# Kernel optimization log

Measured on AMD Instinct MI355X. Metric: run time of the kernel, lower is better.

The kernel has to match this reference:

```python
import jax, jax.numpy as jnp
import numpy as np

N = 2048        # rows of input (nodes / samples)
D_IN = 1024     # input_dim
D_OUT = 8192    # output_dim == number of rows/cols of sparse adj
E = 131072      # nnz of adj (avg degree 16 over D_OUT)


def setup_inputs() -> dict:
    key = jax.random.key(0)
    k0, k1, k2, k3, k4 = jax.random.split(key, 5)
    inp = jax.random.normal(k0, (N, D_IN), dtype=jnp.float32)
    # kaiming_uniform_ on [D_IN, D_OUT]: bound = sqrt(6 / fan_in)
    bound = float(np.sqrt(6.0 / D_IN))
    weight = jax.random.uniform(k1, (D_IN, D_OUT), dtype=jnp.float32,
                                minval=-bound, maxval=bound)
    bias = jnp.zeros((D_OUT,), dtype=jnp.float32)
    adj_rows = jax.random.randint(k2, (E,), 0, D_OUT, dtype=jnp.int64)
    adj_cols = jax.random.randint(k3, (E,), 0, D_OUT, dtype=jnp.int64)
    adj_vals = jax.random.uniform(k4, (E,), dtype=jnp.float32)
    return {"input": inp, "weight": weight, "bias": bias,
            "adj_rows": adj_rows, "adj_cols": adj_cols, "adj_vals": adj_vals}


def reference(input, weight, bias, adj_rows, adj_cols, adj_vals):
    # support = input @ W                      -> [N, D_OUT]
    support = jnp.matmul(input, weight)
    # torch.sparse.mm(adj, support.T).T == (adj @ support^T)^T,
    # with adj sparse COO [D_OUT, D_OUT]: result[r, :] += val_e * support[:, col_e]
    support_t = support.T                      # [D_OUT, N]
    msgs = adj_vals[:, None] * support_t[adj_cols]          # [E, N]
    agg = jax.ops.segment_sum(msgs, adj_rows, num_segments=D_OUT)  # [D_OUT, N]
    return agg.T + bias                        # [N, D_OUT]
```

## Files before the change

### kernel.cpp

```cpp
#include <hip/hip_runtime.h>
#include <hip/hip_bf16.h>


#define N_ROWS 2048
#define D_IN   1024
#define D_OUT  8192
#define SLOT_SHIFT 6
#define SLOTS (1 << SLOT_SHIFT)

typedef __attribute__((ext_vector_type(8))) short bf16x8;
typedef __attribute__((ext_vector_type(4))) float f32x4;
typedef __attribute__((ext_vector_type(2))) float f32x2;

__device__ __forceinline__ float bf2f(unsigned short u) {
    union { unsigned int i; float f; } x; x.i = ((unsigned int)u) << 16; return x.f;
}
__device__ __forceinline__ unsigned short f2bf(float f) {
    union { unsigned int i; float f; } x; x.f = f;
    unsigned int r = x.i + 0x7FFFu + ((x.i >> 16) & 1u);
    return (unsigned short)(r >> 16);
}

__device__ __forceinline__ void async_load16(const void* g, void* l) {
    __builtin_amdgcn_global_load_lds(
        (const __attribute__((address_space(1))) void*)g,
        (__attribute__((address_space(3))) void*)l,
        16, 0, 0);
}

__global__ __launch_bounds__(256) void fused_pre(
    const float* __restrict__ w, unsigned short* __restrict__ wt,
    const float* __restrict__ in, unsigned short* __restrict__ xout,
    const int* __restrict__ rows, const int* __restrict__ cols,
    const float* __restrict__ vals,
    int* __restrict__ cursors, int2* __restrict__ csr_cv, int E)
{
    __shared__ float tile[64][65];
    const int b = blockIdx.x;
    const int t = threadIdx.x;

    if (b < 2048) {
        const int bx = b & 127;
        const int by = b >> 7;
        #pragma unroll
        for (int pass = 0; pass < 4; ++pass) {
            const int item = pass * 256 + t;
            const int r  = item >> 4;
            const int c4 = item & 15;
            const float4 v = *(const float4*)&w[(size_t)(by * 64 + r) * D_OUT + bx * 64 + c4 * 4];
            tile[r][c4 * 4 + 0] = v.x; tile[r][c4 * 4 + 1] = v.y;
            tile[r][c4 * 4 + 2] = v.z; tile[r][c4 * 4 + 3] = v.w;
        }
        __syncthreads();
        #pragma unroll
        for (int pass = 0; pass < 4; ++pass) {
            const int item = pass * 256 + t;
            const int rr  = item >> 4;
            const int cc4 = item & 15;
            ushort4 o;
            o.x = f2bf(tile[cc4 * 4 + 0][rr]);
            o.y = f2bf(tile[cc4 * 4 + 1][rr]);
            o.z = f2bf(tile[cc4 * 4 + 2][rr]);
            o.w = f2bf(tile[cc4 * 4 + 3][rr]);
            *(ushort4*)&wt[(size_t)(bx * 64 + rr) * D_IN + by * 64 + cc4 * 4] = o;
        }
    } else if (b < 4096) {
        const int i = ((b - 2048) * 256 + t) * 4;
        const float4 v = *(const float4*)(in + i);
        ushort4 o; o.x = f2bf(v.x); o.y = f2bf(v.y); o.z = f2bf(v.z); o.w = f2bf(v.w);
        *(ushort4*)(xout + i) = o;
    } else {
        const int e = (b - 4096) * 256 + t;
        if (e < E) {
            const int r = rows[e];
            const int pos = atomicAdd(&cursors[r], 1);
            if (pos < SLOTS) {
                int2 cv; cv.x = cols[e]; cv.y = __float_as_int(vals[e]);
                csr_cv[(r << SLOT_SHIFT) + pos] = cv;
            }
        }
    }
}

__global__ __launch_bounds__(256, 8) void aggregate_slices(
    const unsigned short* __restrict__ wtb,
    const int* __restrict__ cnts,
    const int2* __restrict__ csr_cv,
    unsigned short* __restrict__ wpt)
{
    const int wave  = threadIdx.x >> 6;
    const int lane  = threadIdx.x & 63;
    const int slice = blockIdx.x & 7;
    const int r     = (blockIdx.x >> 3) * 4 + wave;
    const int k0    = slice * 128 + lane * 2;

    const int beg = r << SLOT_SHIFT;
    int cnt = cnts[r]; if (cnt > SLOTS) cnt = SLOTS;
    const int end = beg + cnt;

    const unsigned short* wb = wtb + k0;
    f32x2 acc = (f32x2){0.f, 0.f};

    int i = beg;
    for (; i + 4 <= end; i += 4) {
        int2 cv[4]; unsigned int g[4];
        #pragma unroll
        for (int j = 0; j < 4; ++j) cv[j] = csr_cv[i + j];
        #pragma unroll
        for (int j = 0; j < 4; ++j)
            g[j] = *(const unsigned int*)(wb + (size_t)cv[j].x * D_IN);
        #pragma unroll
        for (int j = 0; j < 4; ++j) {
            const float v = __int_as_float(cv[j].y);
            union { unsigned int i; float f; } lo, hi;
            lo.i = g[j] << 16; hi.i = g[j] & 0xffff0000u;
            acc += (f32x2){v, v} * (f32x2){lo.f, hi.f};
        }
    }
    for (; i < end; ++i) {
        const int2 cv = csr_cv[i];
        const float v = __int_as_float(cv.y);
        const unsigned int g = *(const unsigned int*)(wb + (size_t)cv.x * D_IN);
        union { unsigned int i; float f; } lo, hi;
        lo.i = g << 16; hi.i = g & 0xffff0000u;
        acc += (f32x2){v, v} * (f32x2){lo.f, hi.f};
    }

    const unsigned int o = (unsigned int)f2bf(acc[0]) | ((unsigned int)f2bf(acc[1]) << 16);
    *(unsigned int*)(wpt + (size_t)r * D_IN + k0) = o;
}

struct QuadFrags { bf16x8 a00, a01, a10, a11; };

#define READQ_G(Q, AK, MI0)                                                     \
    (Q).a00 = *(const bf16x8*)((AK) + (MI0)     * 16384);                       \
    (Q).a01 = *(const bf16x8*)((AK) + (MI0)     * 16384 + 32);                  \
    (Q).a10 = *(const bf16x8*)((AK) + (MI0 + 1) * 16384);                       \
    (Q).a11 = *(const bf16x8*)((AK) + (MI0 + 1) * 16384 + 32);

#define READ_BFR(BASE)                                                          \
    _Pragma("unroll")                                                           \
    for (int ni = 0; ni < 4; ++ni) {                                            \
        bfr[0][ni] = *(const bf16x8*)((BASE) + rowB + ni * 1024 + x0 * 8);      \
        bfr[1][ni] = *(const bf16x8*)((BASE) + rowB + ni * 1024 + x1 * 8);      \
    }

#define MFMA_Q(Q, MI0)                                                          \
    __builtin_amdgcn_s_setprio(1);                                              \
    _Pragma("unroll")                                                           \
    for (int ni = 0; ni < 4; ++ni)                                              \
        acc[MI0][ni]     = __builtin_amdgcn_mfma_f32_16x16x32_bf16(             \
            (Q).a00, bfr[0][ni], acc[MI0][ni], 0, 0, 0);                        \
    _Pragma("unroll")                                                           \
    for (int ni = 0; ni < 4; ++ni)                                              \
        acc[MI0 + 1][ni] = __builtin_amdgcn_mfma_f32_16x16x32_bf16(             \
            (Q).a10, bfr[0][ni], acc[MI0 + 1][ni], 0, 0, 0);                    \
    _Pragma("unroll")                                                           \
    for (int ni = 0; ni < 4; ++ni)                                              \
        acc[MI0][ni]     = __builtin_amdgcn_mfma_f32_16x16x32_bf16(             \
            (Q).a01, bfr[1][ni], acc[MI0][ni], 0, 0, 0);                        \
    _Pragma("unroll")                                                           \
    for (int ni = 0; ni < 4; ++ni)                                              \
        acc[MI0 + 1][ni] = __builtin_amdgcn_mfma_f32_16x16x32_bf16(             \
            (Q).a11, bfr[1][ni], acc[MI0 + 1][ni], 0, 0, 0);                    \
    __builtin_amdgcn_s_setprio(0);

__global__ __launch_bounds__(512, 2) void gemm_bt_bias(
    const unsigned short* __restrict__ A,
    const unsigned short* __restrict__ B,
    const float*  __restrict__ bias,
    float* __restrict__ C)
{
    __shared__ unsigned short lds[32768];

    const int tid  = threadIdx.x;
    const int wave = tid >> 6;
    const int lane = tid & 63;
    const int q    = lane >> 4;
    const int l16  = lane & 15;
    const int wr   = wave >> 2;
    const int wc   = wave & 3;

    const int bc = blockIdx.x;
    const int br = blockIdx.y;

    const int srow = tid >> 3;
    const int lc   = (tid & 7) ^ (srow & 7);
    const char* Bsrc = (const char*)B + ((size_t)(bc * 256) + srow) * (D_IN * 2) + lc * 16;
    char* ldsc = (char*)lds;

    const int x0   = q ^ (l16 & 7);
    const int x1   = x0 ^ 4;
    const int rowB = (wc * 64 + l16) * 64;

    const unsigned short* aA =
        A + (size_t)(br * 256 + wr * 128 + l16) * D_IN + q * 8;

    f32x4 acc[8][4];
    #pragma unroll
    for (int i = 0; i < 8; ++i)
        #pragma unroll
        for (int j = 0; j < 4; ++j)
            acc[i][j] = (f32x4){0.f, 0.f, 0.f, 0.f};

    #pragma unroll
    for (int j = 0; j < 4; ++j)
        async_load16(Bsrc + (size_t)j * 64 * (D_IN * 2), ldsc + j * 8192 + tid * 16);

    asm volatile("s_waitcnt vmcnt(0)" ::: "memory");
    __builtin_amdgcn_s_barrier();

    QuadFrags RA, RB;
    bf16x8 bfr[2][4];
    {
        READ_BFR(lds)
        READQ_G(RA, aA, 0)
    }

    for (int kt = 0; kt < D_IN / 64; ++kt) {
        const int cur = kt & 1;
        const unsigned short* Bb = lds + cur * 16384;
        char* dstB = ldsc + (cur ^ 1) * 32768 + tid * 16;
        const char* srcB = Bsrc + (size_t)(kt + 1) * 128;
        const unsigned short* aK = aA + kt * 64;
        const bool pf = (kt + 1 < D_IN / 64);

        if (pf) {
            async_load16(srcB,                            dstB);
            async_load16(srcB + (size_t)64  * (D_IN * 2), dstB + 8192);
            async_load16(srcB + (size_t)128 * (D_IN * 2), dstB + 16384);
            async_load16(srcB + (size_t)192 * (D_IN * 2), dstB + 24576);
        }
        READQ_G(RB, aK, 2)
        MFMA_Q(RA, 0)

        READQ_G(RA, aK, 4)
        MFMA_Q(RB, 2)

        READQ_G(RB, aK, 6)
        MFMA_Q(RA, 4)

        if (pf) {
            asm volatile("s_waitcnt vmcnt(0) lgkmcnt(0)" ::: "memory");
            __builtin_amdgcn_s_barrier();
            READQ_G(RA, aK + 64, 0)
            MFMA_Q(RB, 6)
            READ_BFR(lds + (cur ^ 1) * 16384)
        } else {
            MFMA_Q(RB, 6)
        }
    }

    #pragma unroll
    for (int ni = 0; ni < 4; ++ni) {
        const int col = bc * 256 + wc * 64 + ni * 16 + l16;
        const float bv = bias[col];
        #pragma unroll
        for (int mi = 0; mi < 8; ++mi) {
            const int row0 = br * 256 + wr * 128 + mi * 16 + q * 4;
            #pragma unroll
            for (int r = 0; r < 4; ++r)
                C[(size_t)(row0 + r) * D_OUT + col] = acc[mi][ni][r] + bv;
        }
    }
}

extern "C" void kernel_launch(void* const* d_in, const int* in_sizes, int n_in,
                              void* d_out, int out_size, void* d_ws, size_t ws_size,
                              hipStream_t stream) {
    (void)n_in; (void)out_size; (void)ws_size;
    const float* input    = (const float*)d_in[0];
    const float* weight   = (const float*)d_in[1];
    const float* bias     = (const float*)d_in[2];
    const int*   adj_rows = (const int*)d_in[3];
    const int*   adj_cols = (const int*)d_in[4];
    const float* adj_vals = (const float*)d_in[5];
    const int E = in_sizes[3];

    char* ws = (char*)d_ws;
    unsigned short* wtb = (unsigned short*)ws;
    unsigned short* wpt = (unsigned short*)(ws + (size_t)16 * 1024 * 1024);
    unsigned short* abf = (unsigned short*)(ws + (size_t)32 * 1024 * 1024);
    int*   cursors  = (int*)(ws + (size_t)36 * 1024 * 1024);
    int2*  csr_cv   = (int2*)(ws + (size_t)36 * 1024 * 1024 + 32 * 1024);

    const int fillBlocks = (E + 255) / 256;

    hipMemsetAsync(cursors, 0, D_OUT * sizeof(int), stream);
    fused_pre<<<4096 + fillBlocks, 256, 0, stream>>>(
        weight, wtb, input, abf, adj_rows, adj_cols, adj_vals,
        cursors, csr_cv, E);
    aggregate_slices<<<(D_OUT / 4) * 8, 256, 0, stream>>>(
        wtb, cursors, csr_cv, wpt);
    gemm_bt_bias<<<dim3(D_OUT / 256, N_ROWS / 256), 512, 0, stream>>>(
        abf, wpt, bias, (float*)d_out);
}
```

Before: 220.8 us.

## Stage A and B tiles through a triple-buffered LDS pipeline with K-step 32

The GEMM kernel now loads both the A and B tiles into LDS with async global-to-LDS copies, where before A fragments were read straight from global memory into registers. It uses a three-stage ring buffer with a K-step of 32, prefetching two stages ahead and waiting with vmcnt(4) so copies overlap with the MFMA work. This is meant to remove uncoalesced or latency-exposed global reads of A and to deepen the pipeline. In exchange it uses more LDS (96KB per block, which may limit occupancy to one block per CU at 160KB) and needs a barrier every 32-wide K step, twice as often as before.

```diff
diff --git a/kernel.cpp b/kernel.cpp
--- a/kernel.cpp
+++ b/kernel.cpp
@@ -130,48 +130,13 @@
     *(unsigned int*)(wpt + (size_t)r * D_IN + k0) = o;
 }
 
-struct QuadFrags { bf16x8 a00, a01, a10, a11; };
-
-#define READQ_G(Q, AK, MI0)                                                     \
-    (Q).a00 = *(const bf16x8*)((AK) + (MI0)     * 16384);                       \
-    (Q).a01 = *(const bf16x8*)((AK) + (MI0)     * 16384 + 32);                  \
-    (Q).a10 = *(const bf16x8*)((AK) + (MI0 + 1) * 16384);                       \
-    (Q).a11 = *(const bf16x8*)((AK) + (MI0 + 1) * 16384 + 32);
-
-#define READ_BFR(BASE)                                                          \
-    _Pragma("unroll")                                                           \
-    for (int ni = 0; ni < 4; ++ni) {                                            \
-        bfr[0][ni] = *(const bf16x8*)((BASE) + rowB + ni * 1024 + x0 * 8);      \
-        bfr[1][ni] = *(const bf16x8*)((BASE) + rowB + ni * 1024 + x1 * 8);      \
-    }
-
-#define MFMA_Q(Q, MI0)                                                          \
-    __builtin_amdgcn_s_setprio(1);                                              \
-    _Pragma("unroll")                                                           \
-    for (int ni = 0; ni < 4; ++ni)                                              \
-        acc[MI0][ni]     = __builtin_amdgcn_mfma_f32_16x16x32_bf16(             \
-            (Q).a00, bfr[0][ni], acc[MI0][ni], 0, 0, 0);                        \
-    _Pragma("unroll")                                                           \
-    for (int ni = 0; ni < 4; ++ni)                                              \
-        acc[MI0 + 1][ni] = __builtin_amdgcn_mfma_f32_16x16x32_bf16(             \
-            (Q).a10, bfr[0][ni], acc[MI0 + 1][ni], 0, 0, 0);                    \
-    _Pragma("unroll")                                                           \
-    for (int ni = 0; ni < 4; ++ni)                                              \
-        acc[MI0][ni]     = __builtin_amdgcn_mfma_f32_16x16x32_bf16(             \
-            (Q).a01, bfr[1][ni], acc[MI0][ni], 0, 0, 0);                        \
-    _Pragma("unroll")                                                           \
-    for (int ni = 0; ni < 4; ++ni)                                              \
-        acc[MI0 + 1][ni] = __builtin_amdgcn_mfma_f32_16x16x32_bf16(             \
-            (Q).a11, bfr[1][ni], acc[MI0 + 1][ni], 0, 0, 0);                    \
-    __builtin_amdgcn_s_setprio(0);
-
 __global__ __launch_bounds__(512, 2) void gemm_bt_bias(
     const unsigned short* __restrict__ A,
     const unsigned short* __restrict__ B,
     const float*  __restrict__ bias,
     float* __restrict__ C)
 {
-    __shared__ unsigned short lds[32768];
+    __shared__ unsigned short lds[49152];
 
     const int tid  = threadIdx.x;
     const int wave = tid >> 6;
@@ -184,17 +149,15 @@
     const int bc = blockIdx.x;
     const int br = blockIdx.y;
 
-    const int srow = tid >> 3;
-    const int lc   = (tid & 7) ^ (srow & 7);
+    const int srow = tid >> 2;
+    const int lc   = (tid & 3) ^ (srow & 3);
+    const char* Asrc = (const char*)A + ((size_t)(br * 256) + srow) * (D_IN * 2) + lc * 16;
     const char* Bsrc = (const char*)B + ((size_t)(bc * 256) + srow) * (D_IN * 2) + lc * 16;
     char* ldsc = (char*)lds;
 
-    const int x0   = q ^ (l16 & 7);
-    const int x1   = x0 ^ 4;
-    const int rowB = (wc * 64 + l16) * 64;
-
-    const unsigned short* aA =
-        A + (size_t)(br * 256 + wr * 128 + l16) * D_IN + q * 8;
+    const int xc   = (q ^ (l16 & 3)) * 8;
+    const int rowA = (wr * 128 + l16) * 32;
+    const int rowB = (wc * 64  + l16) * 32;
 
     f32x4 acc[8][4];
     #pragma unroll
@@ -203,53 +166,51 @@
         for (int j = 0; j < 4; ++j)
             acc[i][j] = (f32x4){0.f, 0.f, 0.f, 0.f};
 
-    #pragma unroll
-    for (int j = 0; j < 4; ++j)
-        async_load16(Bsrc + (size_t)j * 64 * (D_IN * 2), ldsc + j * 8192 + tid * 16);
-
-    asm volatile("s_waitcnt vmcnt(0)" ::: "memory");
-    __builtin_amdgcn_s_barrier();
-
-    QuadFrags RA, RB;
-    bf16x8 bfr[2][4];
-    {
-        READ_BFR(lds)
-        READQ_G(RA, aA, 0)
-    }
-
-    for (int kt = 0; kt < D_IN / 64; ++kt) {
-        const int cur = kt & 1;
-        const unsigned short* Bb = lds + cur * 16384;
-        char* dstB = ldsc + (cur ^ 1) * 32768 + tid * 16;
-        const char* srcB = Bsrc + (size_t)(kt + 1) * 128;
-        const unsigned short* aK = aA + kt * 64;
-        const bool pf = (kt + 1 < D_IN / 64);
-
-        if (pf) {
-            async_load16(srcB,                            dstB);
-            async_load16(srcB + (size_t)64  * (D_IN * 2), dstB + 8192);
-            async_load16(srcB + (size_t)128 * (D_IN * 2), dstB + 16384);
-            async_load16(srcB + (size_t)192 * (D_IN * 2), dstB + 24576);
-        }
-        READQ_G(RB, aK, 2)
-        MFMA_Q(RA, 0)
-
-        READQ_G(RA, aK, 4)
-        MFMA_Q(RB, 2)
-
-        READQ_G(RB, aK, 6)
-        MFMA_Q(RA, 4)
-
-        if (pf) {
-            asm volatile("s_waitcnt vmcnt(0) lgkmcnt(0)" ::: "memory");
-            __builtin_amdgcn_s_barrier();
-            READQ_G(RA, aK + 64, 0)
-            MFMA_Q(RB, 6)
-            READ_BFR(lds + (cur ^ 1) * 16384)
-        } else {
-            MFMA_Q(RB, 6)
-        }
-    }
+    #define STAGE(T, BUF)                                                   \
+    {   const size_t ko = (size_t)(T) * 64;                                 \
+        char* d = ldsc + (BUF) * 32768 + tid * 16;                          \
+        async_load16(Asrc + ko,                          d);                \
+        async_load16(Asrc + (size_t)128 * (D_IN * 2) + ko, d + 8192);       \
+        async_load16(Bsrc + ko,                          d + 16384);        \
+        async_load16(Bsrc + (size_t)128 * (D_IN * 2) + ko, d + 24576);  }
+
+    STAGE(0, 0)
+    STAGE(1, 1)
+
+    int b0 = 0;
+    for (int t = 0; t < 32; ++t) {
+        if (t < 31) asm volatile("s_waitcnt vmcnt(4) lgkmcnt(0)" ::: "memory");
+        else        asm volatile("s_waitcnt vmcnt(0) lgkmcnt(0)" ::: "memory");
+        __builtin_amdgcn_s_barrier();
+
+        if (t + 2 < 32) {
+            int b2 = b0 + 2; if (b2 >= 3) b2 -= 3;
+            STAGE(t + 2, b2)
+        }
+
+        const unsigned short* Ab = lds + b0 * 16384;
+        const unsigned short* Bb = Ab + 8192;
+
+        bf16x8 bfv[4], afv[8];
+        #pragma unroll
+        for (int ni = 0; ni < 4; ++ni)
+            bfv[ni] = *(const bf16x8*)(Bb + rowB + ni * 512 + xc);
+        #pragma unroll
+        for (int mi = 0; mi < 8; ++mi)
+            afv[mi] = *(const bf16x8*)(Ab + rowA + mi * 512 + xc);
+
+        __builtin_amdgcn_s_setprio(1);
+        #pragma unroll
+        for (int mi = 0; mi < 8; ++mi)
+            #pragma unroll
+            for (int ni = 0; ni < 4; ++ni)
+                acc[mi][ni] = __builtin_amdgcn_mfma_f32_16x16x32_bf16(
+                    afv[mi], bfv[ni], acc[mi][ni], 0, 0, 0);
+        __builtin_amdgcn_s_setprio(0);
+
+        b0 = (b0 == 2) ? 0 : b0 + 1;
+    }
+    #undef STAGE
 
     #pragma unroll
     for (int ni = 0; ni < 4; ++ni) {
```

New measurement: 183.2 us. 17.0% less time.
